# Kernel tuning notes

Hardware: AMD Instinct MI355X
Metric: run time of the kernel (lower is better)

Reference implementation:

```python
import jax, jax.numpy as jnp
import numpy as np

FEAT_STRIDE = 16
PRE_NMS, POST_NMS, NMS_THRESH = 6000, 300, 0.7  # state == 'test'

# ---- anchor generation (numpy, done once) ----

def _whctrs(a):
    w = a[2] - a[0] + 1.0
    h = a[3] - a[1] + 1.0
    return w, h, a[0] + 0.5 * (w - 1.0), a[1] + 0.5 * (h - 1.0)

def _mkanchors(ws, hs, xc, yc):
    return np.stack([xc - 0.5 * (ws - 1.0), yc - 0.5 * (hs - 1.0),
                     xc + 0.5 * (ws - 1.0), yc + 0.5 * (hs - 1.0)], axis=1)

def generate_anchors(base_size, scales, ratios):
    base = np.array([0.0, 0.0, base_size - 1.0, base_size - 1.0], np.float64)
    w, h, xc, yc = _whctrs(base)
    size = w * h
    ws = np.round(np.sqrt(size / ratios))
    hs = np.round(ws * ratios)
    ratio_anchors = _mkanchors(ws, hs, xc, yc)
    out = []
    for i in range(ratio_anchors.shape[0]):
        w, h, xc, yc = _whctrs(ratio_anchors[i])
        out.append(_mkanchors(w * scales, h * scales, xc, yc))
    return np.concatenate(out, 0).astype(np.float32)  # [9, 4]

# ---- box utilities ----

def bbox_transform_inv(anchors, deltas):
    widths = anchors[..., 2] - anchors[..., 0] + 1.0
    heights = anchors[..., 3] - anchors[..., 1] + 1.0
    cx = anchors[..., 0] + 0.5 * widths
    cy = anchors[..., 1] + 0.5 * heights
    dx, dy, dw, dh = deltas[..., 0], deltas[..., 1], deltas[..., 2], deltas[..., 3]
    pcx = dx * widths + cx
    pcy = dy * heights + cy
    pw = jnp.exp(dw) * widths
    ph = jnp.exp(dh) * heights
    return jnp.stack([pcx - 0.5 * pw, pcy - 0.5 * ph,
                      pcx + 0.5 * pw, pcy + 0.5 * ph], axis=-1)

def clip_boxes(boxes, img_info):
    # img_info = [height, width]
    x1 = jnp.clip(boxes[..., 0], 0.0, img_info[1] - 1.0)
    y1 = jnp.clip(boxes[..., 1], 0.0, img_info[0] - 1.0)
    x2 = jnp.clip(boxes[..., 2], 0.0, img_info[1] - 1.0)
    y2 = jnp.clip(boxes[..., 3], 0.0, img_info[0] - 1.0)
    return jnp.stack([x1, y1, x2, y2], axis=-1)

def nms_keep(boxes, thresh):
    # boxes [N,4], already sorted by score descending; returns bool keep mask [N]
    n = boxes.shape[0]
    x1, y1, x2, y2 = boxes[:, 0], boxes[:, 1], boxes[:, 2], boxes[:, 3]
    areas = (x2 - x1 + 1.0) * (y2 - y1 + 1.0)
    xx1 = jnp.maximum(x1[:, None], x1[None, :])
    yy1 = jnp.maximum(y1[:, None], y1[None, :])
    xx2 = jnp.minimum(x2[:, None], x2[None, :])
    yy2 = jnp.minimum(y2[:, None], y2[None, :])
    inter = jnp.maximum(0.0, xx2 - xx1 + 1.0) * jnp.maximum(0.0, yy2 - yy1 + 1.0)
    iou = inter / (areas[:, None] + areas[None, :] - inter)  # [N,N]
    over = iou > thresh
    idxs = jnp.arange(n)
    def step(suppressed, i):
        kept = jnp.logical_not(suppressed[i])
        suppressed = suppressed | (kept & over[i] & (idxs > i))
        return suppressed, kept
    _, keep = jax.lax.scan(step, jnp.zeros(n, bool), idxs)
    return keep


def setup_inputs() -> dict:
    key = jax.random.key(0)
    k1, k2 = jax.random.split(key)
    B, H, W = 4, 64, 64
    scores = jax.random.normal(k1, (B, 18, H, W), dtype=jnp.float32)
    bbox_deltas = jax.random.normal(k2, (B, 36, H, W), dtype=jnp.float32)
    img_info = jnp.array([H * FEAT_STRIDE, W * FEAT_STRIDE], dtype=jnp.float32)
    anchors = jnp.asarray(generate_anchors(FEAT_STRIDE,
                                           np.array([8.0, 16.0, 32.0]),
                                           np.array([0.5, 1.0, 2.0])))
    return {"scores": scores, "bbox_deltas": bbox_deltas,
            "img_info": img_info, "anchors": anchors}


def reference(scores, bbox_deltas, img_info, anchors):
    B = scores.shape[0]
    A = anchors.shape[0]
    fg = scores[:, A:]                       # [B, A, H, W] foreground scores
    H, W = fg.shape[2], fg.shape[3]
    sx = jnp.arange(W, dtype=scores.dtype) * FEAT_STRIDE
    sy = jnp.arange(H, dtype=scores.dtype) * FEAT_STRIDE
    gx, gy = jnp.meshgrid(sx, sy)            # 'xy' indexing -> [H, W]
    shifts = jnp.stack([gx.ravel(), gy.ravel(), gx.ravel(), gy.ravel()], -1)  # [K,4]
    all_anchors = (anchors[None] + shifts[:, None]).reshape(-1, 4)            # [K*A,4]
    scs = fg.transpose(0, 2, 3, 1).reshape(B, -1)                # [B, K*A]
    deltas = bbox_deltas.transpose(0, 2, 3, 1).reshape(B, -1, 4)  # [B, K*A, 4]
    props = bbox_transform_inv(all_anchors[None], deltas)
    props = clip_boxes(props, img_info)

    def per_image(args):
        p, s = args
        _, order = jax.lax.top_k(s, PRE_NMS)          # descending score order
        b = p[order]                                   # [PRE_NMS, 4]
        keep = nms_keep(b, NMS_THRESH)
        idx = jnp.where(keep, size=POST_NMS, fill_value=-1)[0]
        valid = (idx >= 0).astype(b.dtype)
        sel = b[jnp.maximum(idx, 0)] * valid[:, None]  # zero-pad missing rows
        return sel                                      # [POST_NMS, 4]

    sel = jax.lax.map(per_image, (props, scs))          # [B, POST_NMS, 4]
    bidx = jnp.broadcast_to(jnp.arange(B, dtype=sel.dtype)[:, None, None],
                            (B, POST_NMS, 1))
    return jnp.concatenate([bidx, sel], axis=-1)        # [B, POST_NMS, 5]
```

## Files before the change

kernel.cpp:

```cpp
#include <hip/hip_runtime.h>
#include <stdint.h>

#define HH 64
#define WW 64
#define AA 9
#define N_PER (HH*WW*AA)
#define NB 4
#define PRE_NMS 6000
#define POST_NMS 300
#define NMS_THRESH 0.7f
#define FEAT_STRIDE 16
#define M 1024
#define MW 16
#define BINS 65536
#define KSHIFT 48
#define SCAT_MAX 8000

#define OFF_TOPB   0u
#define OFF_MSK    393216u
#define OFF_H      917504u
#define OFF_SS     1966080u
#define OFF_CUR    3014656u
#define OFF_B1     4063232u
#define OFF_NSEL   4063248u
#define OFF_SCAT   4063264u

__device__ __forceinline__ uint64_t make_key(const float* __restrict__ scores, int b, int j) {
    int a = j >> 12, hw = j & 4095;
    float sc = scores[((size_t)b*18 + 9 + a)*4096 + hw];
    uint32_t u = __float_as_uint(sc);
    u = (u & 0x80000000u) ? ~u : (u | 0x80000000u);
    uint32_t i = (uint32_t)(hw*9 + a);
    return ((uint64_t)u << 32) | (uint32_t)(~i);
}

__global__ void __launch_bounds__(1024) hist_kernel(const float* __restrict__ scores,
                                                    uint32_t* __restrict__ Hg) {
    int tid = blockIdx.x*1024 + threadIdx.x;
    int b = tid / N_PER;
    int j = tid - b*N_PER;
    uint64_t k64 = make_key(scores, b, j);
    atomicAdd(&Hg[(uint32_t)b*BINS + (uint32_t)(k64 >> KSHIFT)], 1u);
}

__global__ void __launch_bounds__(1024) scan_cutoff(const uint32_t* __restrict__ Hg,
                                                    uint32_t* __restrict__ SSg,
                                                    uint32_t* __restrict__ CURg,
                                                    uint32_t* __restrict__ B1g,
                                                    uint32_t* __restrict__ NselG) {
    int b = blockIdx.x;
    int t = threadIdx.x;
    __shared__ uint32_t blksum[1024];
    __shared__ int shB1;
    __shared__ uint32_t shNsel;

    uint32_t base = (uint32_t)t * 64u;
    const uint32_t* Hb = Hg + (size_t)b*BINS;
    uint32_t loc[64];
    uint32_t lsum = 0;
    #pragma unroll
    for (int k = 0; k < 16; ++k) {
        uint4 v = ((const uint4*)(Hb + base))[k];
        loc[4*k+0] = v.x; loc[4*k+1] = v.y; loc[4*k+2] = v.z; loc[4*k+3] = v.w;
        lsum += v.x + v.y + v.z + v.w;
    }
    blksum[t] = lsum;
    __syncthreads();
    for (int off = 1; off < 1024; off <<= 1) {
        uint32_t add = (t + off < 1024) ? blksum[t + off] : 0u;
        __syncthreads();
        blksum[t] += add;
        __syncthreads();
    }
    uint32_t run = (t < 1023) ? blksum[t + 1] : 0u;
    #pragma unroll
    for (int k = 63; k >= 0; --k) { uint32_t h = loc[k]; loc[k] = run; run += h; }
    #pragma unroll
    for (int k = 0; k < 64; ++k) {
        uint32_t ss   = loc[k];
        uint32_t prev = (k == 0) ? blksum[t] : loc[k-1];
        if (ss < PRE_NMS && prev >= PRE_NMS) { shB1 = (int)(base + (uint32_t)k); shNsel = prev; }
    }
    __syncthreads();
    int B1 = shB1;
    if (t == 0) { B1g[b] = (uint32_t)B1; NselG[b] = shNsel; }
    uint32_t* SSb  = SSg  + (size_t)b*BINS;
    uint32_t* CURb = CURg + (size_t)b*BINS;
    if ((int)base >= B1) {
        #pragma unroll
        for (int k = 0; k < 16; ++k) {
            uint4 v = make_uint4(loc[4*k+0], loc[4*k+1], loc[4*k+2], loc[4*k+3]);
            ((uint4*)(SSb + base))[k]  = v;
            ((uint4*)(CURb + base))[k] = v;
        }
    } else if ((int)(base + 63u) >= B1) {
        #pragma unroll
        for (int k = 0; k < 64; ++k) {
            if ((int)(base + (uint32_t)k) >= B1) {
                SSb[base + k]  = loc[k];
                CURb[base + k] = loc[k];
            }
        }
    }
}

__global__ void __launch_bounds__(1024) scatter_kernel(const float* __restrict__ scores,
                                                       const uint32_t* __restrict__ B1g,
                                                       uint32_t* __restrict__ CURg,
                                                       uint64_t* __restrict__ scatG) {
    int tid = blockIdx.x*1024 + threadIdx.x;
    int b = tid / N_PER;
    int j = tid - b*N_PER;
    uint64_t k64 = make_key(scores, b, j);
    uint32_t bin = (uint32_t)(k64 >> KSHIFT);
    if (bin >= B1g[b]) {
        uint32_t slot = atomicAdd(&CURg[(uint32_t)b*BINS + bin], 1u);
        if (slot < SCAT_MAX) scatG[(uint32_t)b*SCAT_MAX + slot] = k64;
    }
}

__global__ void __launch_bounds__(1024) rank_decode(const uint64_t* __restrict__ scatG,
                                                    const uint32_t* __restrict__ SSg,
                                                    const uint32_t* __restrict__ CURg,
                                                    const uint32_t* __restrict__ NselG,
                                                    const float* __restrict__ deltas,
                                                    const float* __restrict__ img_info,
                                                    const float* __restrict__ anchors,
                                                    float* __restrict__ topb) {
#pragma clang fp contract(off)
    int b = blockIdx.y;
    uint32_t s = blockIdx.x*1024u + threadIdx.x;
    uint32_t n = min(NselG[b], (uint32_t)SCAT_MAX);
    if (s >= n) return;
    const uint64_t* sg = scatG + (uint32_t)b*SCAT_MAX;
    uint64_t k64 = sg[s];
    uint32_t bin = (uint32_t)(k64 >> KSHIFT);
    uint32_t start = SSg[(uint32_t)b*BINS + bin];
    uint32_t end = min(CURg[(uint32_t)b*BINS + bin], (uint32_t)SCAT_MAX);
    uint32_t cnt = 0;
    uint32_t j = start;
    for (; j + 4 <= end; j += 4) {
        uint64_t a0 = sg[j], a1 = sg[j+1], a2 = sg[j+2], a3 = sg[j+3];
        cnt += (a0 > k64) ? 1u : 0u;
        cnt += (a1 > k64) ? 1u : 0u;
        cnt += (a2 > k64) ? 1u : 0u;
        cnt += (a3 > k64) ? 1u : 0u;
    }
    for (; j < end; ++j) cnt += (sg[j] > k64) ? 1u : 0u;
    uint32_t r = start + cnt;
    if (r >= PRE_NMS) return;

    uint32_t i = ~(uint32_t)(k64 & 0xFFFFFFFFu);
    int a = (int)(i % 9u);
    int hw = (int)(i / 9u);
    int h = hw >> 6, w = hw & 63;
    float sx = (float)(w * FEAT_STRIDE);
    float sy = (float)(h * FEAT_STRIDE);
    float ax1 = anchors[a*4+0] + sx;
    float ay1 = anchors[a*4+1] + sy;
    float ax2 = anchors[a*4+2] + sx;
    float ay2 = anchors[a*4+3] + sy;
    float width  = ax2 - ax1 + 1.0f;
    float height = ay2 - ay1 + 1.0f;
    float cx = ax1 + 0.5f * width;
    float cy = ay1 + 0.5f * height;
    size_t dbase = ((size_t)b*36 + a*4) * 4096 + hw;
    float dx = deltas[dbase];
    float dy = deltas[dbase + 4096];
    float dw = deltas[dbase + 2*4096];
    float dh = deltas[dbase + 3*4096];
    float pcx = dx * width + cx;
    float pcy = dy * height + cy;
    float pw = (float)exp((double)dw) * width;
    float ph = (float)exp((double)dh) * height;
    float x1 = pcx - 0.5f * pw;
    float y1 = pcy - 0.5f * ph;
    float x2 = pcx + 0.5f * pw;
    float y2 = pcy + 0.5f * ph;
    float maxx = img_info[1] - 1.0f;
    float maxy = img_info[0] - 1.0f;
    x1 = fminf(fmaxf(x1, 0.0f), maxx);
    y1 = fminf(fmaxf(y1, 0.0f), maxy);
    x2 = fminf(fmaxf(x2, 0.0f), maxx);
    y2 = fminf(fmaxf(y2, 0.0f), maxy);
    *(float4*)(topb + ((size_t)b*PRE_NMS + r)*4) = make_float4(x1, y1, x2, y2);
}

__global__ void __launch_bounds__(64) nms_mask_small(const float* __restrict__ topb,
                                                     uint64_t* __restrict__ msk) {
#pragma clang fp contract(off)
    int jblock = blockIdx.x;
    int iblock = blockIdx.y;
    int b = blockIdx.z;
    int t = threadIdx.x;
    __shared__ float4 jb[64];
    __shared__ float jarea[64];
    int j0 = jblock*64;
    {
        float4 bj = *(const float4*)(topb + ((size_t)b*PRE_NMS + j0 + t)*4);
        jb[t] = bj;
        jarea[t] = (bj.z - bj.x + 1.0f) * (bj.w - bj.y + 1.0f);
    }
    __syncthreads();
    int i = iblock*64 + t;
    float4 bi = *(const float4*)(topb + ((size_t)b*PRE_NMS + i)*4);
    float areai = (bi.z - bi.x + 1.0f) * (bi.w - bi.y + 1.0f);
    uint64_t bits = 0;
    for (int jj = 0; jj < 64; ++jj) {
        float4 bj = jb[jj];
        float xx1 = fmaxf(bi.x, bj.x);
        float yy1 = fmaxf(bi.y, bj.y);
        float xx2 = fminf(bi.z, bj.z);
        float yy2 = fminf(bi.w, bj.w);
        float iw = fmaxf(0.0f, xx2 - xx1 + 1.0f);
        float ih = fmaxf(0.0f, yy2 - yy1 + 1.0f);
        float inter = iw * ih;
        float iou = inter / ((areai + jarea[jj]) - inter);
        if (iou > NMS_THRESH) bits |= (1ull << jj);
    }
    msk[((size_t)b*M + i)*MW + jblock] = bits;
}

__global__ void __launch_bounds__(64) nms_scan_lds(const uint64_t* __restrict__ msk,
                                                   const float* __restrict__ topb,
                                                   float* __restrict__ out) {
#pragma clang fp contract(off)
    int b = blockIdx.x;
    int l = threadIdx.x;
    __shared__ __align__(16) uint64_t rows[M][MW];
    __shared__ int keepL[POST_NMS];
    __shared__ float skx1[POST_NMS], sky1[POST_NMS], skx2[POST_NMS], sky2[POST_NMS], skar[POST_NMS];

    const uint8_t* src0 = (const uint8_t*)(msk + (size_t)b*M*MW);
    uint8_t* dst0 = (uint8_t*)&rows[0][0];
    for (int it = 0; it < (M*MW*8)/1024; ++it) {
        __builtin_amdgcn_global_load_lds(
            (const __attribute__((address_space(1))) uint32_t*)(src0 + it*1024 + l*16),
            (__attribute__((address_space(3))) uint32_t*)(dst0 + it*1024 + l*16),
            16, 0, 0);
    }
    asm volatile("s_waitcnt vmcnt(0)" ::: "memory");
    __builtin_amdgcn_sched_barrier(0);

    uint64_t remv = 0ull;
    int nkeep = 0;
    int cur = 0;
    bool exhausted = false;
    while (true) {
        if (l == 0) keepL[nkeep] = cur;
        nkeep++;
        if (nkeep >= POST_NMS) break;
        uint64_t rw = (l < MW) ? rows[cur][l] : 0ull;
        remv |= rw;
        uint64_t live = (l < MW) ? ~remv : 0ull;
        int local = live ? (l*64 + (int)__builtin_ctzll(live)) : 0x7FFFFFFF;
        uint64_t mb = __ballot(live != 0ull);
        if (mb == 0ull) { exhausted = true; break; }
        cur = __builtin_amdgcn_readlane(local, (int)__builtin_ctzll(mb));
    }

    if (nkeep < POST_NMS && exhausted) {
        for (int k = l; k < nkeep; k += 64) {
            float4 bx = *(const float4*)(topb + ((size_t)b*PRE_NMS + keepL[k])*4);
            skx1[k] = bx.x; sky1[k] = bx.y; skx2[k] = bx.z; sky2[k] = bx.w;
            skar[k] = (bx.z - bx.x + 1.0f) * (bx.w - bx.y + 1.0f);
        }
        int base = M;
        while (nkeep < POST_NMS && base < PRE_NMS) {
            int c = base + l;
            float4 bc = make_float4(0.f, 0.f, 0.f, 0.f);
            bool sup = true;
            if (c < PRE_NMS) {
                bc = *(const float4*)(topb + ((size_t)b*PRE_NMS + c)*4);
                sup = false;
            }
            float ac = (bc.z - bc.x + 1.0f) * (bc.w - bc.y + 1.0f);
            for (int k = 0; k < nkeep; ++k) {
                float xx1 = fmaxf(skx1[k], bc.x);
                float yy1 = fmaxf(sky1[k], bc.y);
                float xx2 = fminf(skx2[k], bc.z);
                float yy2 = fminf(sky2[k], bc.w);
                float iw = fmaxf(0.0f, xx2 - xx1 + 1.0f);
                float ih = fmaxf(0.0f, yy2 - yy1 + 1.0f);
                float inter = iw * ih;
                float iou = inter / ((skar[k] + ac) - inter);
                if (iou > NMS_THRESH) sup = true;
            }
            uint64_t live = __ballot(!sup);
            while (live != 0ull && nkeep < POST_NMS) {
                int j = (int)__builtin_ctzll(live);
                int cj = base + j;
                if (l == 0) keepL[nkeep] = cj;
                float jx1 = __shfl(bc.x, j);
                float jy1 = __shfl(bc.y, j);
                float jx2 = __shfl(bc.z, j);
                float jy2 = __shfl(bc.w, j);
                float ja  = __shfl(ac, j);
                if (l == 0) { skx1[nkeep]=jx1; sky1[nkeep]=jy1; skx2[nkeep]=jx2; sky2[nkeep]=jy2; skar[nkeep]=ja; }
                nkeep++;
                float xx1 = fmaxf(jx1, bc.x);
                float yy1 = fmaxf(jy1, bc.y);
                float xx2 = fminf(jx2, bc.z);
                float yy2 = fminf(jy2, bc.w);
                float iw = fmaxf(0.0f, xx2 - xx1 + 1.0f);
                float ih = fmaxf(0.0f, yy2 - yy1 + 1.0f);
                float inter = iw * ih;
                float iou = inter / ((ja + ac) - inter);
                uint64_t kill = __ballot(iou > NMS_THRESH);
                live &= ~kill;
                live &= ~(1ull << j);
            }
            base += 64;
        }
    }
    __syncthreads();

    for (int k = l; k < POST_NMS; k += 64) {
        float* o = out + ((size_t)b*POST_NMS + k)*5;
        o[0] = (float)b;
        if (k < nkeep) {
            float4 bx = *(const float4*)(topb + ((size_t)b*PRE_NMS + keepL[k])*4);
            o[1] = bx.x; o[2] = bx.y; o[3] = bx.z; o[4] = bx.w;
        } else {
            o[1] = 0.0f; o[2] = 0.0f; o[3] = 0.0f; o[4] = 0.0f;
        }
    }
}

extern "C" void kernel_launch(void* const* d_in, const int* in_sizes, int n_in,
                              void* d_out, int out_size, void* d_ws, size_t ws_size,
                              hipStream_t stream) {
    const float* scores   = (const float*)d_in[0];
    const float* deltas   = (const float*)d_in[1];
    const float* img_info = (const float*)d_in[2];
    const float* anchors  = (const float*)d_in[3];
    float* out = (float*)d_out;

    uint8_t* ws = (uint8_t*)d_ws;
    float*    topb  = (float*)(ws + OFF_TOPB);
    uint64_t* msk   = (uint64_t*)(ws + OFF_MSK);
    uint32_t* Hg    = (uint32_t*)(ws + OFF_H);
    uint32_t* SSg   = (uint32_t*)(ws + OFF_SS);
    uint32_t* CURg  = (uint32_t*)(ws + OFF_CUR);
    uint32_t* B1g   = (uint32_t*)(ws + OFF_B1);
    uint32_t* NselG = (uint32_t*)(ws + OFF_NSEL);
    uint64_t* scatG = (uint64_t*)(ws + OFF_SCAT);

    hipMemsetAsync(Hg, 0, (size_t)NB*BINS*4, stream);

    hist_kernel<<<(NB*N_PER)/1024, 1024, 0, stream>>>(scores, Hg);
    scan_cutoff<<<NB, 1024, 0, stream>>>(Hg, SSg, CURg, B1g, NselG);
    scatter_kernel<<<(NB*N_PER)/1024, 1024, 0, stream>>>(scores, B1g, CURg, scatG);
    rank_decode<<<dim3(SCAT_MAX/1000, NB), 1024, 0, stream>>>(scatG, SSg, CURg, NselG,
                                                              deltas, img_info, anchors, topb);

    dim3 mg(MW, MW, NB);
    nms_mask_small<<<mg, 64, 0, stream>>>(topb, msk);

    nms_scan_lds<<<NB, 64, 0, stream>>>(msk, topb, out);
}
```

Baseline: 172.9 us.

## Widen NMS scan load to four waves and prefetch predicted next mask row

The NMS scan kernel now launches 256 threads so four waves share the global-to-LDS copy of the suppression mask. A __syncthreads makes the data visible, and only the first wave then runs the serial scan. Inside the scan, the wave speculatively computes the candidate that would follow the current pick and loads its mask row early. When the prediction holds, the LDS read latency leaves the serial dependency chain. This adds an extra ballot and readlane per iteration plus a wasted load whenever the prediction misses.

```diff
diff --git a/kernel.cpp b/kernel.cpp
--- a/kernel.cpp
+++ b/kernel.cpp
@@ -221,108 +221,129 @@
     msk[((size_t)b*M + i)*MW + jblock] = bits;
 }
 
-__global__ void __launch_bounds__(64) nms_scan_lds(const uint64_t* __restrict__ msk,
-                                                   const float* __restrict__ topb,
-                                                   float* __restrict__ out) {
+__global__ void __launch_bounds__(256) nms_scan_lds(const uint64_t* __restrict__ msk,
+                                                    const float* __restrict__ topb,
+                                                    float* __restrict__ out) {
 #pragma clang fp contract(off)
     int b = blockIdx.x;
-    int l = threadIdx.x;
+    int tid = threadIdx.x;
+    int wid = tid >> 6, lane = tid & 63;
     __shared__ __align__(16) uint64_t rows[M][MW];
     __shared__ int keepL[POST_NMS];
     __shared__ float skx1[POST_NMS], sky1[POST_NMS], skx2[POST_NMS], sky2[POST_NMS], skar[POST_NMS];
 
     const uint8_t* src0 = (const uint8_t*)(msk + (size_t)b*M*MW);
     uint8_t* dst0 = (uint8_t*)&rows[0][0];
-    for (int it = 0; it < (M*MW*8)/1024; ++it) {
+    for (int c = wid; c < (M*MW*8)/1024; c += 4) {
         __builtin_amdgcn_global_load_lds(
-            (const __attribute__((address_space(1))) uint32_t*)(src0 + it*1024 + l*16),
-            (__attribute__((address_space(3))) uint32_t*)(dst0 + it*1024 + l*16),
+            (const __attribute__((address_space(1))) uint32_t*)(src0 + c*1024 + lane*16),
+            (__attribute__((address_space(3))) uint32_t*)(dst0 + c*1024 + lane*16),
             16, 0, 0);
     }
     asm volatile("s_waitcnt vmcnt(0)" ::: "memory");
     __builtin_amdgcn_sched_barrier(0);
-
-    uint64_t remv = 0ull;
-    int nkeep = 0;
-    int cur = 0;
-    bool exhausted = false;
-    while (true) {
-        if (l == 0) keepL[nkeep] = cur;
-        nkeep++;
-        if (nkeep >= POST_NMS) break;
-        uint64_t rw = (l < MW) ? rows[cur][l] : 0ull;
-        remv |= rw;
-        uint64_t live = (l < MW) ? ~remv : 0ull;
-        int local = live ? (l*64 + (int)__builtin_ctzll(live)) : 0x7FFFFFFF;
-        uint64_t mb = __ballot(live != 0ull);
-        if (mb == 0ull) { exhausted = true; break; }
-        cur = __builtin_amdgcn_readlane(local, (int)__builtin_ctzll(mb));
-    }
-
-    if (nkeep < POST_NMS && exhausted) {
-        for (int k = l; k < nkeep; k += 64) {
-            float4 bx = *(const float4*)(topb + ((size_t)b*PRE_NMS + keepL[k])*4);
-            skx1[k] = bx.x; sky1[k] = bx.y; skx2[k] = bx.z; sky2[k] = bx.w;
-            skar[k] = (bx.z - bx.x + 1.0f) * (bx.w - bx.y + 1.0f);
-        }
-        int base = M;
-        while (nkeep < POST_NMS && base < PRE_NMS) {
-            int c = base + l;
-            float4 bc = make_float4(0.f, 0.f, 0.f, 0.f);
-            bool sup = true;
-            if (c < PRE_NMS) {
-                bc = *(const float4*)(topb + ((size_t)b*PRE_NMS + c)*4);
-                sup = false;
-            }
-            float ac = (bc.z - bc.x + 1.0f) * (bc.w - bc.y + 1.0f);
-            for (int k = 0; k < nkeep; ++k) {
-                float xx1 = fmaxf(skx1[k], bc.x);
-                float yy1 = fmaxf(sky1[k], bc.y);
-                float xx2 = fminf(skx2[k], bc.z);
-                float yy2 = fminf(sky2[k], bc.w);
-                float iw = fmaxf(0.0f, xx2 - xx1 + 1.0f);
-                float ih = fmaxf(0.0f, yy2 - yy1 + 1.0f);
-                float inter = iw * ih;
-                float iou = inter / ((skar[k] + ac) - inter);
-                if (iou > NMS_THRESH) sup = true;
-            }
-            uint64_t live = __ballot(!sup);
-            while (live != 0ull && nkeep < POST_NMS) {
-                int j = (int)__builtin_ctzll(live);
-                int cj = base + j;
-                if (l == 0) keepL[nkeep] = cj;
-                float jx1 = __shfl(bc.x, j);
-                float jy1 = __shfl(bc.y, j);
-                float jx2 = __shfl(bc.z, j);
-                float jy2 = __shfl(bc.w, j);
-                float ja  = __shfl(ac, j);
-                if (l == 0) { skx1[nkeep]=jx1; sky1[nkeep]=jy1; skx2[nkeep]=jx2; sky2[nkeep]=jy2; skar[nkeep]=ja; }
-                nkeep++;
-                float xx1 = fmaxf(jx1, bc.x);
-                float yy1 = fmaxf(jy1, bc.y);
-                float xx2 = fminf(jx2, bc.z);
-                float yy2 = fminf(jy2, bc.w);
-                float iw = fmaxf(0.0f, xx2 - xx1 + 1.0f);
-                float ih = fmaxf(0.0f, yy2 - yy1 + 1.0f);
-                float inter = iw * ih;
-                float iou = inter / ((ja + ac) - inter);
-                uint64_t kill = __ballot(iou > NMS_THRESH);
-                live &= ~kill;
-                live &= ~(1ull << j);
-            }
-            base += 64;
-        }
-    }
     __syncthreads();
 
-    for (int k = l; k < POST_NMS; k += 64) {
-        float* o = out + ((size_t)b*POST_NMS + k)*5;
-        o[0] = (float)b;
-        if (k < nkeep) {
-            float4 bx = *(const float4*)(topb + ((size_t)b*PRE_NMS + keepL[k])*4);
-            o[1] = bx.x; o[2] = bx.y; o[3] = bx.z; o[4] = bx.w;
-        } else {
-            o[1] = 0.0f; o[2] = 0.0f; o[3] = 0.0f; o[4] = 0.0f;
+    if (tid < 64) {
+        int l = lane;
+        uint64_t remv = 0ull;
+        int nkeep = 0;
+        int cur = 0;
+        bool exhausted = false;
+
+        uint64_t rvN = (l < MW) ? rows[0][l] : 0ull;
+        int pred = 1;
+        uint64_t rvP = (l < MW) ? rows[1][l] : 0ull;
+
+        while (true) {
+            if (l == 0) keepL[nkeep] = cur;
+            nkeep++;
+            if (nkeep >= POST_NMS) break;
+            remv |= rvN;
+            uint64_t live = (l < MW) ? ~remv : 0ull;
+            int local = live ? (l*64 + (int)__builtin_ctzll(live)) : 0x7FFFFFFF;
+            uint64_t mb = __ballot(live != 0ull);
+            if (mb == 0ull) { exhausted = true; break; }
+            int next = __builtin_amdgcn_readlane(local, (int)__builtin_ctzll(mb));
+            if (next == pred) {
+                rvN = rvP;
+            } else {
+                rvN = (l < MW) ? rows[next][l] : 0ull;
+            }
+            uint64_t live2 = live;
+            if (l == (next >> 6)) live2 &= ~(1ull << (next & 63));
+            int local2 = live2 ? (l*64 + (int)__builtin_ctzll(live2)) : 0x7FFFFFFF;
+            uint64_t mb2 = __ballot(live2 != 0ull);
+            int p2 = (mb2 != 0ull) ? __builtin_amdgcn_readlane(local2, (int)__builtin_ctzll(mb2)) : next;
+            pred = p2;
+            rvP = (l < MW) ? rows[p2][l] : 0ull;
+            cur = next;
+        }
+
+        if (nkeep < POST_NMS && exhausted) {
+            for (int k = l; k < nkeep; k += 64) {
+                float4 bx = *(const float4*)(topb + ((size_t)b*PRE_NMS + keepL[k])*4);
+                skx1[k] = bx.x; sky1[k] = bx.y; skx2[k] = bx.z; sky2[k] = bx.w;
+                skar[k] = (bx.z - bx.x + 1.0f) * (bx.w - bx.y + 1.0f);
+            }
+            int base = M;
+            while (nkeep < POST_NMS && base < PRE_NMS) {
+                int c = base + l;
+                float4 bc = make_float4(0.f, 0.f, 0.f, 0.f);
+                bool sup = true;
+                if (c < PRE_NMS) {
+                    bc = *(const float4*)(topb + ((size_t)b*PRE_NMS + c)*4);
+                    sup = false;
+                }
+                float ac = (bc.z - bc.x + 1.0f) * (bc.w - bc.y + 1.0f);
+                for (int k = 0; k < nkeep; ++k) {
+                    float xx1 = fmaxf(skx1[k], bc.x);
+                    float yy1 = fmaxf(sky1[k], bc.y);
+                    float xx2 = fminf(skx2[k], bc.z);
+                    float yy2 = fminf(sky2[k], bc.w);
+                    float iw = fmaxf(0.0f, xx2 - xx1 + 1.0f);
+                    float ih = fmaxf(0.0f, yy2 - yy1 + 1.0f);
+                    float inter = iw * ih;
+                    float iou = inter / ((skar[k] + ac) - inter);
+                    if (iou > NMS_THRESH) sup = true;
+                }
+                uint64_t live = __ballot(!sup);
+                while (live != 0ull && nkeep < POST_NMS) {
+                    int j = (int)__builtin_ctzll(live);
+                    int cj = base + j;
+                    if (l == 0) keepL[nkeep] = cj;
+                    float jx1 = __shfl(bc.x, j);
+                    float jy1 = __shfl(bc.y, j);
+                    float jx2 = __shfl(bc.z, j);
+                    float jy2 = __shfl(bc.w, j);
+                    float ja  = __shfl(ac, j);
+                    if (l == 0) { skx1[nkeep]=jx1; sky1[nkeep]=jy1; skx2[nkeep]=jx2; sky2[nkeep]=jy2; skar[nkeep]=ja; }
+                    nkeep++;
+                    float xx1 = fmaxf(jx1, bc.x);
+                    float yy1 = fmaxf(jy1, bc.y);
+                    float xx2 = fminf(jx2, bc.z);
+                    float yy2 = fminf(jy2, bc.w);
+                    float iw = fmaxf(0.0f, xx2 - xx1 + 1.0f);
+                    float ih = fmaxf(0.0f, yy2 - yy1 + 1.0f);
+                    float inter = iw * ih;
+                    float iou = inter / ((ja + ac) - inter);
+                    uint64_t kill = __ballot(iou > NMS_THRESH);
+                    live &= ~kill;
+                    live &= ~(1ull << j);
+                }
+                base += 64;
+            }
+        }
+
+        for (int k = l; k < POST_NMS; k += 64) {
+            float* o = out + ((size_t)b*POST_NMS + k)*5;
+            o[0] = (float)b;
+            if (k < nkeep) {
+                float4 bx = *(const float4*)(topb + ((size_t)b*PRE_NMS + keepL[k])*4);
+                o[1] = bx.x; o[2] = bx.y; o[3] = bx.z; o[4] = bx.w;
+            } else {
+                o[1] = 0.0f; o[2] = 0.0f; o[3] = 0.0f; o[4] = 0.0f;
+            }
         }
     }
 }
@@ -357,5 +378,5 @@
     dim3 mg(MW, MW, NB);
     nms_mask_small<<<mg, 64, 0, stream>>>(topb, msk);
 
-    nms_scan_lds<<<NB, 64, 0, stream>>>(msk, topb, out);
-}
+    nms_scan_lds<<<NB, 256, 0, stream>>>(msk, topb, out);
+}
```

Measured after the change: 191.4 us. 1.11x slower.
